# Kernel optimization log

Hardware: AMD Instinct MI355X
Metric: run time of the kernel (lower is better)

The kernel has to match this reference:

```python
import jax, jax.numpy as jnp
import numpy as np
from jax import lax


def setup_inputs() -> dict:
    key = jax.random.key(0)
    N_b, N_s = 256, 131072
    input_attenuation = jax.random.normal(key, (N_b, N_s), dtype=jnp.float32)
    return {"input_attenuation": input_attenuation, "k_steps": 64}


def reference(input_attenuation, k_steps):
    # Causal sliding-window minimum: out[b, i] = min(x[b, max(0, i-k+1) : i+1]).
    # Single fused reduce_window pass; left-pad (k-1) with +inf (identity of min).
    return lax.reduce_window(
        input_attenuation,
        jnp.inf,
        lax.min,
        window_dimensions=(1, k_steps),
        window_strides=(1, 1),
        padding=((0, 0), (k_steps - 1, 0)),
    )
```

## Files before the change

### kernel.cpp

```cpp
#include <hip/hip_runtime.h>


constexpr int N_S = 131072;
constexpr int TILE = 256;
constexpr int SEG_TILES = 16;
constexpr int SEG = TILE * SEG_TILES;

__global__ __launch_bounds__(256) void swmin64_kernel(const float* __restrict__ in,
                                                      float* __restrict__ out,
                                                      int n_rows) {
    const int lane = threadIdx.x & 63;
    const int wave_in_blk = threadIdx.x >> 6;
    const long long wave_id = (long long)blockIdx.x * 4 + wave_in_blk;
    const int segs_per_row = N_S / SEG;
    const int row = (int)(wave_id / segs_per_row);
    const int seg = (int)(wave_id % segs_per_row);
    if (row >= n_rows) return;

    const float INF = __builtin_huge_valf();
    const float* rp = in + (long long)row * N_S + (long long)seg * SEG;
    float* wp = out + (long long)row * N_S + (long long)seg * SEG;

    float c0 = INF, c1 = INF, c2 = INF, c3 = INF;

    if (seg != 0) {
        const float4 v = *(const float4*)(rp - TILE + 4 * lane);
        float s3 = v.w;
        float s2 = fminf(v.z, s3);
        float s1 = fminf(v.y, s2);
        float s0 = fminf(v.x, s1);
        float m = s0;
        float es = __shfl_down(m, 1, 16);
        if ((lane & 15) == 15) es = INF;
        es = fminf(es, __shfl_down(es, 1, 16));
        es = fminf(es, __shfl_down(es, 2, 16));
        es = fminf(es, __shfl_down(es, 4, 16));
        es = fminf(es, __shfl_down(es, 8, 16));
        float S0 = fminf(es, s0), S1 = fminf(es, s1), S2 = fminf(es, s2), S3 = fminf(es, s3);
        c0 = __shfl_down(S1, 48);
        c1 = __shfl_down(S2, 48);
        c2 = __shfl_down(S3, 48);
        c3 = __shfl_down(S0, 49);
    }

    for (int it = 0; it < SEG_TILES; ++it) {
        const float4 v = *(const float4*)(rp + it * TILE + 4 * lane);

        float p0 = v.x, p1 = fminf(p0, v.y), p2 = fminf(p1, v.z), p3 = fminf(p2, v.w);
        float s3 = v.w, s2 = fminf(v.z, s3), s1 = fminf(v.y, s2), s0 = fminf(v.x, s1);
        float m = s0;

        float ep = __shfl_up(m, 1, 16);
        if ((lane & 15) == 0) ep = INF;
        ep = fminf(ep, __shfl_up(ep, 1, 16));
        ep = fminf(ep, __shfl_up(ep, 2, 16));
        ep = fminf(ep, __shfl_up(ep, 4, 16));
        ep = fminf(ep, __shfl_up(ep, 8, 16));

        float es = __shfl_down(m, 1, 16);
        if ((lane & 15) == 15) es = INF;
        es = fminf(es, __shfl_down(es, 1, 16));
        es = fminf(es, __shfl_down(es, 2, 16));
        es = fminf(es, __shfl_down(es, 4, 16));
        es = fminf(es, __shfl_down(es, 8, 16));

        float P0 = fminf(ep, p0), P1 = fminf(ep, p1), P2 = fminf(ep, p2), P3 = fminf(ep, p3);
        float S0 = fminf(es, s0), S1 = fminf(es, s1), S2 = fminf(es, s2), S3 = fminf(es, s3);

        float u0 = __shfl_up(S1, 16);
        float u1 = __shfl_up(S2, 16);
        float u2 = __shfl_up(S3, 16);
        float u3 = __shfl_up(S0, 15);
        float T0 = (lane >= 16) ? u0 : c0;
        float T1 = (lane >= 16) ? u1 : c1;
        float T2 = (lane >= 16) ? u2 : c2;
        float T3 = (lane >= 15) ? u3 : c3;

        float4 o;
        o.x = fminf(P0, T0);
        o.y = fminf(P1, T1);
        o.z = fminf(P2, T2);
        o.w = fminf(P3, T3);
        *(float4*)(wp + it * TILE + 4 * lane) = o;

        c0 = __shfl_down(S1, 48);
        c1 = __shfl_down(S2, 48);
        c2 = __shfl_down(S3, 48);
        c3 = __shfl_down(S0, 49);
    }
}

extern "C" void kernel_launch(void* const* d_in, const int* in_sizes, int n_in,
                              void* d_out, int out_size, void* d_ws, size_t ws_size,
                              hipStream_t stream) {
    const float* in = (const float*)d_in[0];
    float* out = (float*)d_out;
    const int total = in_sizes[0];
    const int n_rows = total / N_S;
    const int waves = n_rows * (N_S / SEG);
    const int blocks = waves / 4;
    swmin64_kernel<<<blocks, 256, 0, stream>>>(in, out, n_rows);
}
```

Baseline: 51.21 us.

## Use DPP row shifts and merged bpermute for scans, prefetch next tile

The 16-lane prefix and suffix min scans now use DPP row-shift intrinsics instead of generic shuffles. A single ds_bpermute with a rotated address serves both the cross-row shift within the tile and the carry into the next tile, replacing separate shfl_up and shfl_down calls. The tile loop is fully unrolled and software-pipelined so the next tile's load is issued before the current one is processed. This cuts LDS-based shuffle traffic and hides global load latency, at the cost of more registers.

```diff
diff --git a/kernel.cpp b/kernel.cpp
--- a/kernel.cpp
+++ b/kernel.cpp
@@ -5,6 +5,85 @@
 constexpr int TILE = 256;
 constexpr int SEG_TILES = 16;
 constexpr int SEG = TILE * SEG_TILES;
+
+#define ROW_SHL(n) (0x100 | (n))
+#define ROW_SHR(n) (0x110 | (n))
+
+template <int CTRL>
+__device__ __forceinline__ float dpp_shift_inf(float x) {
+    int t = __builtin_amdgcn_update_dpp(0x7f800000, __float_as_int(x), CTRL, 0xf, 0xf, false);
+    return __int_as_float(t);
+}
+
+template <int CTRL>
+__device__ __forceinline__ float dpp_min(float x) {
+    int xi = __float_as_int(x);
+    int t = __builtin_amdgcn_update_dpp(xi, xi, CTRL, 0xf, 0xf, false);
+    return fminf(x, __int_as_float(t));
+}
+
+__device__ __forceinline__ float bperm(int addr, float v) {
+    return __int_as_float(__builtin_amdgcn_ds_bpermute(addr, __float_as_int(v)));
+}
+
+__device__ __forceinline__ void tile_S(const float4 v, float& S0, float& S1, float& S2,
+                                       float& S3) {
+    float s3 = v.w;
+    float s2 = fminf(v.z, s3);
+    float s1 = fminf(v.y, s2);
+    float s0 = fminf(v.x, s1);
+    float es = dpp_shift_inf<ROW_SHL(1)>(s0);
+    es = dpp_min<ROW_SHL(1)>(es);
+    es = dpp_min<ROW_SHL(2)>(es);
+    es = dpp_min<ROW_SHL(4)>(es);
+    es = dpp_min<ROW_SHL(8)>(es);
+    S0 = fminf(es, s0);
+    S1 = fminf(es, s1);
+    S2 = fminf(es, s2);
+    S3 = fminf(es, s3);
+}
+
+__device__ __forceinline__ void process_tile(const float4 v, int lane, int a16, int a15,
+                                             float& c0, float& c1, float& c2, float& c3,
+                                             float* dst) {
+    float p0 = v.x, p1 = fminf(p0, v.y), p2 = fminf(p1, v.z), p3 = fminf(p2, v.w);
+    float s3 = v.w, s2 = fminf(v.z, s3), s1 = fminf(v.y, s2), s0 = fminf(v.x, s1);
+
+    float ep = dpp_shift_inf<ROW_SHR(1)>(s0);
+    ep = dpp_min<ROW_SHR(1)>(ep);
+    ep = dpp_min<ROW_SHR(2)>(ep);
+    ep = dpp_min<ROW_SHR(4)>(ep);
+    ep = dpp_min<ROW_SHR(8)>(ep);
+    float es = dpp_shift_inf<ROW_SHL(1)>(s0);
+    es = dpp_min<ROW_SHL(1)>(es);
+    es = dpp_min<ROW_SHL(2)>(es);
+    es = dpp_min<ROW_SHL(4)>(es);
+    es = dpp_min<ROW_SHL(8)>(es);
+
+    float P0 = fminf(ep, p0), P1 = fminf(ep, p1), P2 = fminf(ep, p2), P3 = fminf(ep, p3);
+    float S0 = fminf(es, s0), S1 = fminf(es, s1), S2 = fminf(es, s2), S3 = fminf(es, s3);
+
+    float r0 = bperm(a16, S1);
+    float r1 = bperm(a16, S2);
+    float r2 = bperm(a16, S3);
+    float r3 = bperm(a15, S0);
+
+    float T0 = (lane >= 16) ? r0 : c0;
+    float T1 = (lane >= 16) ? r1 : c1;
+    float T2 = (lane >= 16) ? r2 : c2;
+    float T3 = (lane >= 15) ? r3 : c3;
+    c0 = r0;
+    c1 = r1;
+    c2 = r2;
+    c3 = r3;
+
+    float4 o;
+    o.x = fminf(P0, T0);
+    o.y = fminf(P1, T1);
+    o.z = fminf(P2, T2);
+    o.w = fminf(P3, T3);
+    *(float4*)dst = o;
+}
 
 __global__ __launch_bounds__(256) void swmin64_kernel(const float* __restrict__ in,
                                                       float* __restrict__ out,
@@ -21,73 +100,31 @@
     const float* rp = in + (long long)row * N_S + (long long)seg * SEG;
     float* wp = out + (long long)row * N_S + (long long)seg * SEG;
 
+    const int a16 = ((lane + 48) & 63) << 2;
+    const int a15 = ((lane + 49) & 63) << 2;
+
     float c0 = INF, c1 = INF, c2 = INF, c3 = INF;
 
+    float4 v = *(const float4*)(rp + 4 * lane);
+
     if (seg != 0) {
-        const float4 v = *(const float4*)(rp - TILE + 4 * lane);
-        float s3 = v.w;
-        float s2 = fminf(v.z, s3);
-        float s1 = fminf(v.y, s2);
-        float s0 = fminf(v.x, s1);
-        float m = s0;
-        float es = __shfl_down(m, 1, 16);
-        if ((lane & 15) == 15) es = INF;
-        es = fminf(es, __shfl_down(es, 1, 16));
-        es = fminf(es, __shfl_down(es, 2, 16));
-        es = fminf(es, __shfl_down(es, 4, 16));
-        es = fminf(es, __shfl_down(es, 8, 16));
-        float S0 = fminf(es, s0), S1 = fminf(es, s1), S2 = fminf(es, s2), S3 = fminf(es, s3);
-        c0 = __shfl_down(S1, 48);
-        c1 = __shfl_down(S2, 48);
-        c2 = __shfl_down(S3, 48);
-        c3 = __shfl_down(S0, 49);
+        const float4 w = *(const float4*)(rp - TILE + 4 * lane);
+        float S0, S1, S2, S3;
+        tile_S(w, S0, S1, S2, S3);
+        c0 = bperm(a16, S1);
+        c1 = bperm(a16, S2);
+        c2 = bperm(a16, S3);
+        c3 = bperm(a15, S0);
     }
 
-    for (int it = 0; it < SEG_TILES; ++it) {
-        const float4 v = *(const float4*)(rp + it * TILE + 4 * lane);
-
-        float p0 = v.x, p1 = fminf(p0, v.y), p2 = fminf(p1, v.z), p3 = fminf(p2, v.w);
-        float s3 = v.w, s2 = fminf(v.z, s3), s1 = fminf(v.y, s2), s0 = fminf(v.x, s1);
-        float m = s0;
-
-        float ep = __shfl_up(m, 1, 16);
-        if ((lane & 15) == 0) ep = INF;
-        ep = fminf(ep, __shfl_up(ep, 1, 16));
-        ep = fminf(ep, __shfl_up(ep, 2, 16));
-        ep = fminf(ep, __shfl_up(ep, 4, 16));
-        ep = fminf(ep, __shfl_up(ep, 8, 16));
-
-        float es = __shfl_down(m, 1, 16);
-        if ((lane & 15) == 15) es = INF;
-        es = fminf(es, __shfl_down(es, 1, 16));
-        es = fminf(es, __shfl_down(es, 2, 16));
-        es = fminf(es, __shfl_down(es, 4, 16));
-        es = fminf(es, __shfl_down(es, 8, 16));
-
-        float P0 = fminf(ep, p0), P1 = fminf(ep, p1), P2 = fminf(ep, p2), P3 = fminf(ep, p3);
-        float S0 = fminf(es, s0), S1 = fminf(es, s1), S2 = fminf(es, s2), S3 = fminf(es, s3);
-
-        float u0 = __shfl_up(S1, 16);
-        float u1 = __shfl_up(S2, 16);
-        float u2 = __shfl_up(S3, 16);
-        float u3 = __shfl_up(S0, 15);
-        float T0 = (lane >= 16) ? u0 : c0;
-        float T1 = (lane >= 16) ? u1 : c1;
-        float T2 = (lane >= 16) ? u2 : c2;
-        float T3 = (lane >= 15) ? u3 : c3;
-
-        float4 o;
-        o.x = fminf(P0, T0);
-        o.y = fminf(P1, T1);
-        o.z = fminf(P2, T2);
-        o.w = fminf(P3, T3);
-        *(float4*)(wp + it * TILE + 4 * lane) = o;
-
-        c0 = __shfl_down(S1, 48);
-        c1 = __shfl_down(S2, 48);
-        c2 = __shfl_down(S3, 48);
-        c3 = __shfl_down(S0, 49);
+#pragma unroll
+    for (int it = 0; it < SEG_TILES - 1; ++it) {
+        float4 vn = *(const float4*)(rp + (it + 1) * TILE + 4 * lane);
+        process_tile(v, lane, a16, a15, c0, c1, c2, c3, wp + it * TILE + 4 * lane);
+        v = vn;
     }
+    process_tile(v, lane, a16, a15, c0, c1, c2, c3,
+                 wp + (SEG_TILES - 1) * TILE + 4 * lane);
 }
 
 extern "C" void kernel_launch(void* const* d_in, const int* in_sizes, int n_in,
```

Result: faster. 47.21 us (-7.8%).
